# Performance work log

Measured on AMD Instinct MI355X. Metric: run time of the kernel, lower is better.

## Reference

```python
import jax, jax.numpy as jnp
import numpy as np

B, P_SIDE, ENC = 32, 14, 2048
EMB = DEC = ATT = 512
V, L = 10000, 52


def setup_inputs() -> dict:
    key = jax.random.key(0)
    ks = jax.random.split(key, 16)
    u = lambda k, s, a=0.1: jax.random.uniform(k, s, jnp.float32, -a, a)
    return dict(
        image_features=jax.random.normal(ks[0], (B, P_SIDE, P_SIDE, ENC), jnp.float32),
        caption_tokens=jax.random.randint(ks[1], (B, L), 0, V),
        caption_lengths=jax.random.randint(ks[2], (B,), 2, L + 1).at[0].set(L),
        # Attention (init_weights: uniform(-0.1,0.1), zero bias)
        W_enc=u(ks[3], (ATT, ENC)), b_enc=jnp.zeros((ATT,), jnp.float32),
        W_dec=u(ks[4], (ATT, DEC)), b_dec=jnp.zeros((ATT,), jnp.float32),
        w_full=u(ks[5], (ATT,)), b_full=jnp.zeros((), jnp.float32),
        emb_table=u(ks[6], (V, EMB)),
        # LSTMCell (PyTorch gate order i,f,g,o)
        W_ih=u(ks[7], (4 * DEC, EMB + ENC), 0.02), b_ih=jnp.zeros((4 * DEC,), jnp.float32),
        W_hh=u(ks[8], (4 * DEC, DEC), 0.02), b_hh=jnp.zeros((4 * DEC,), jnp.float32),
        W_h0=u(ks[9], (DEC, ENC), 0.02), b_h0=jnp.zeros((DEC,), jnp.float32),
        W_c0=u(ks[10], (DEC, ENC), 0.02), b_c0=jnp.zeros((DEC,), jnp.float32),
        W_beta=u(ks[11], (ENC, DEC), 0.02), b_beta=jnp.zeros((ENC,), jnp.float32),
        W_fc=u(ks[12], (V, DEC), 0.02), b_fc=jnp.zeros((V,), jnp.float32),
    )


def reference(image_features, caption_tokens, caption_lengths,
              W_enc, b_enc, W_dec, b_dec, w_full, b_full, emb_table,
              W_ih, b_ih, W_hh, b_hh, W_h0, b_h0, W_c0, b_c0,
              W_beta, b_beta, W_fc, b_fc):
    bsz = image_features.shape[0]
    enc_dim = image_features.shape[-1]
    img = image_features.reshape(bsz, -1, enc_dim)            # B,P,ENC
    # sort by caption length descending (torch: caption_lengths.sort(descending=True))
    sort_index = jnp.argsort(-caption_lengths)
    lengths = caption_lengths[sort_index]
    img = img[sort_index]
    toks = caption_tokens[sort_index]
    embs = emb_table[toks]                                    # B,L,EMB
    mean_img = img.mean(axis=1)                               # B,ENC
    h0 = mean_img @ W_h0.T + b_h0
    c0 = mean_img @ W_c0.T + b_c0
    decode_lengths = lengths - 1                              # B
    T = toks.shape[1] - 1                                     # static max decode length
    # encoder projection is h-independent: hoist out of the time loop (same math)
    enc_att = jnp.einsum('bpe,ae->bpa', img, W_enc) + b_enc   # B,P,A

    def step(carry, xs):
        h, c = carry
        emb_t, t = xs                                         # emb_t: B,EMB
        # Bahdanau additive attention
        dec_att = h @ W_dec.T + b_dec                         # B,A
        score = jnp.einsum('bpa,a->bp', jax.nn.relu(enc_att + dec_att[:, None, :]), w_full) + b_full
        alpha = jax.nn.softmax(score, axis=1)                 # B,P
        awe = jnp.einsum('bp,bpe->be', alpha, img)            # B,ENC
        gate = jax.nn.sigmoid(h @ W_beta.T + b_beta)
        awe = gate * awe
        # LSTMCell step on [emb; awe]
        x = jnp.concatenate([emb_t, awe], axis=1)
        g = x @ W_ih.T + b_ih + h @ W_hh.T + b_hh
        gi, gf, gg, go = jnp.split(g, 4, axis=1)
        c_new = jax.nn.sigmoid(gf) * c + jax.nn.sigmoid(gi) * jnp.tanh(gg)
        h_new = jax.nn.sigmoid(go) * jnp.tanh(c_new)
        # dynamic batch truncation -> masking (rows with t >= decode_length freeze)
        active = (t < decode_lengths)[:, None]
        h = jnp.where(active, h_new, h)
        c = jnp.where(active, c_new, c)
        preds = jnp.where(active, h_new @ W_fc.T + b_fc, 0.0)  # dropout in eval = identity
        alpha = jnp.where(active, alpha, 0.0)
        return (h, c), (preds, alpha)

    xs = (jnp.swapaxes(embs[:, :T, :], 0, 1), jnp.arange(T))
    (_, _), (preds, alphas) = jax.lax.scan(step, (h0, c0), xs)
    predictions = jnp.swapaxes(preds, 0, 1)                   # B,T,V
    alphas = jnp.swapaxes(alphas, 0, 1)                       # B,T,P
    return predictions, toks, decode_lengths, alphas, sort_index
```

## Files before the change

kernel.cpp:

```cpp
#include <hip/hip_runtime.h>
#include <hip/hip_bf16.h>
#include <cstddef>

#define BB 32
#define PP 196
#define ENCD 2048
#define EMBD 512
#define DECD 512
#define ATTD 512
#define VV 10000
#define LLEN 52
#define TT 51
#define HPC 8
#define GAC 16

#define OFF_PRED  0
#define OFF_TOKS  16320000
#define OFF_DLEN  16321664
#define OFF_ALPHA 16321696
#define OFF_SIDX  16641568

typedef __attribute__((ext_vector_type(8))) short short8;
typedef __attribute__((ext_vector_type(4))) float floatx4;

__device__ __forceinline__ float sigmf(float x) { return 1.0f / (1.0f + __expf(-x)); }
__device__ __forceinline__ unsigned short f2bf(float x) {
    __hip_bfloat16 h = __float2bfloat16(x);
    return *(unsigned short*)&h;
}

__global__ void k_sort(const int* __restrict__ toks, const int* __restrict__ lens,
                       int* __restrict__ sidx, int* __restrict__ dlen, float* __restrict__ out) {
    __shared__ int s_idx[BB];
    if (threadIdx.x == 0) {
        int idx[BB], ln[BB];
        for (int i = 0; i < BB; i++) { idx[i] = i; ln[i] = lens[i]; }
        for (int i = 1; i < BB; i++) {
            int ci = idx[i], cl = ln[i]; int j = i - 1;
            while (j >= 0 && ln[j] < cl) { ln[j + 1] = ln[j]; idx[j + 1] = idx[j]; j--; }
            ln[j + 1] = cl; idx[j + 1] = ci;
        }
        for (int i = 0; i < BB; i++) {
            s_idx[i] = idx[i];
            sidx[i] = idx[i];
            int d = ln[i] - 1;
            dlen[i] = d;
            out[OFF_DLEN + i] = (float)d;
            out[OFF_SIDX + i] = (float)idx[i];
        }
    }
    __syncthreads();
    for (int i = threadIdx.x; i < BB * LLEN; i += blockDim.x) {
        int b = i / LLEN, l = i % LLEN;
        out[OFF_TOKS + i] = (float)toks[s_idx[b] * LLEN + l];
    }
}

__global__ void k_mean(const float* __restrict__ img, const int* __restrict__ sidx,
                       float* __restrict__ meanT) {
    int b = blockIdx.x, ec = blockIdx.y, tid = threadIdx.x;
    int e = ec * 256 + tid;
    const float* ib = img + (size_t)sidx[b] * PP * ENCD + e;
    float acc = 0.f;
#pragma unroll 4
    for (int p = 0; p < PP; p++) acc += ib[(size_t)p * ENCD];
    meanT[(size_t)e * BB + b] = acc * (1.0f / 196.0f);
}

__global__ void k_h0c0(const float* __restrict__ meanT,
                       const float* __restrict__ Wh0, const float* __restrict__ bh0,
                       const float* __restrict__ Wc0, const float* __restrict__ bc0,
                       float* __restrict__ xT, float* __restrict__ c) {
    __shared__ float sx[256 * BB];
    int tid = threadIdx.x;
    int cl = tid >> 3, bq = tid & 7;
    int col = blockIdx.x * 32 + cl;
    const float* wr = (col < 512) ? Wh0 + (size_t)col * ENCD
                                  : Wc0 + (size_t)(col - 512) * ENCD;
    float acc[4] = {0, 0, 0, 0};
    for (int k0 = 0; k0 < ENCD; k0 += 256) {
        __syncthreads();
        for (int i = tid; i < 256 * BB; i += 256) sx[i] = meanT[(size_t)k0 * BB + i];
        __syncthreads();
        for (int k = 0; k < 256; k++) {
            float w = wr[k0 + k];
            const float* x = sx + k * BB + bq * 4;
            acc[0] += w * x[0]; acc[1] += w * x[1]; acc[2] += w * x[2]; acc[3] += w * x[3];
        }
    }
#pragma unroll
    for (int j = 0; j < 4; j++) {
        int b = bq * 4 + j;
        if (col < 512) {
            float v = acc[j] + bh0[col];
            xT[(size_t)(2048 + col) * BB + b] = v;
        } else {
            float v = acc[j] + bc0[col - 512];
            c[b * DECD + (col - 512)] = v;
        }
    }
}

__global__ void k_twh2(const float* __restrict__ Wdec, const float* __restrict__ Wbeta,
                       const float* __restrict__ Whh, float* __restrict__ WhT2) {
    __shared__ float sT[32][33];
    int kt = blockIdx.x, ct = blockIdx.y;
    int tx = threadIdx.x & 31, ty = threadIdx.x >> 5;
    for (int j = 0; j < 4; j++) {
        int cc = ct * 32 + ty + j * 8;
        int kk = kt * 32 + tx;
        float v = (cc < 512) ? Wdec[(size_t)cc * 512 + kk]
                 : (cc < 2560) ? Wbeta[(size_t)(cc - 512) * 512 + kk]
                               : Whh[(size_t)(cc - 2560) * 512 + kk];
        sT[ty + j * 8][tx] = v;
    }
    __syncthreads();
    for (int j = 0; j < 4; j++) {
        int kk = kt * 32 + ty + j * 8;
        int cc = ct * 32 + tx;
        WhT2[(size_t)kk * 4608 + cc] = sT[tx][ty + j * 8];
    }
}

__global__ void k_twg2(const float* __restrict__ Wih, float* __restrict__ WgaT) {
    __shared__ float sT[32][33];
    int kt = blockIdx.x, dt = blockIdx.y;
    int tx = threadIdx.x & 31, ty = threadIdx.x >> 5;
    for (int j = 0; j < 4; j++) {
        int dd = dt * 32 + ty + j * 8;
        int kk = kt * 32 + tx;
        sT[ty + j * 8][tx] = Wih[(size_t)dd * 2560 + 512 + kk];
    }
    __syncthreads();
    for (int j = 0; j < 4; j++) {
        int kk = kt * 32 + ty + j * 8;
        int dd = dt * 32 + tx;
        WgaT[(size_t)kk * 2048 + dd] = sT[tx][ty + j * 8];
    }
}

__global__ void k_cvtfc(const float* __restrict__ Wfc, unsigned int* __restrict__ WfcB) {
    int base = (blockIdx.x * 256 + threadIdx.x) * 4;
    for (int j = 0; j < 4; j++) {
        int ui = base + j;
        const float* src = Wfc + (size_t)ui * 2;
        unsigned int lo = f2bf(src[0]), hi = f2bf(src[1]);
        WfcB[ui] = lo | (hi << 16);
    }
}

__global__ void k_enc(const float* __restrict__ img, const int* __restrict__ sidx,
                      const float* __restrict__ Wenc, const float* __restrict__ benc,
                      float* __restrict__ enc_att) {
    __shared__ float sA[16][68];
    __shared__ float sW[16][132];
    __shared__ size_t sRB[64];
    int mb = blockIdx.x, c0 = blockIdx.y * 128;
    int tid = threadIdx.x;
    int tm = tid >> 5, tn = tid & 31;
    if (tid < 64) {
        int row = mb * 64 + tid;
        int b = row / PP, p = row % PP;
        sRB[tid] = ((size_t)sidx[b] * PP + p) * ENCD;
    }
    __syncthreads();
    float acc[8][4];
#pragma unroll
    for (int i = 0; i < 8; i++)
#pragma unroll
        for (int j = 0; j < 4; j++) acc[i][j] = 0.f;

    for (int kk = 0; kk < ENCD; kk += 16) {
        {
            int m = tid >> 2, kq = tid & 3;
            float4 v = *(const float4*)(img + sRB[m] + kk + kq * 4);
            sA[kq * 4 + 0][m] = v.x; sA[kq * 4 + 1][m] = v.y;
            sA[kq * 4 + 2][m] = v.z; sA[kq * 4 + 3][m] = v.w;
        }
        {
            int nl = tid & 127, kh = tid >> 7;
            const float* wr = Wenc + (size_t)(c0 + nl) * ENCD + kk + kh * 8;
            float4 v0 = *(const float4*)(wr);
            float4 v1 = *(const float4*)(wr + 4);
            sW[kh * 8 + 0][nl] = v0.x; sW[kh * 8 + 1][nl] = v0.y;
            sW[kh * 8 + 2][nl] = v0.z; sW[kh * 8 + 3][nl] = v0.w;
            sW[kh * 8 + 4][nl] = v1.x; sW[kh * 8 + 5][nl] = v1.y;
            sW[kh * 8 + 6][nl] = v1.z; sW[kh * 8 + 7][nl] = v1.w;
        }
        __syncthreads();
#pragma unroll
        for (int k = 0; k < 16; k++) {
            float4 a0 = *(const float4*)&sA[k][tm * 8];
            float4 a1 = *(const float4*)&sA[k][tm * 8 + 4];
            float4 w0 = *(const float4*)&sW[k][tn * 4];
            float av[8] = {a0.x, a0.y, a0.z, a0.w, a1.x, a1.y, a1.z, a1.w};
            float wv[4] = {w0.x, w0.y, w0.z, w0.w};
#pragma unroll
            for (int i = 0; i < 8; i++)
#pragma unroll
                for (int j = 0; j < 4; j++) acc[i][j] += av[i] * wv[j];
        }
        __syncthreads();
    }
#pragma unroll
    for (int i = 0; i < 8; i++) {
        int row = mb * 64 + tm * 8 + i;
        float* orow = enc_att + (size_t)row * ATTD + c0;
        int ca = tn * 4;
        float4 oa = {acc[i][0] + benc[c0 + ca + 0], acc[i][1] + benc[c0 + ca + 1],
                     acc[i][2] + benc[c0 + ca + 2], acc[i][3] + benc[c0 + ca + 3]};
        *(float4*)(orow + ca) = oa;
    }
}

__global__ void k_gemb(const float* __restrict__ emb, const int* __restrict__ toks,
                       const int* __restrict__ sidx, const float* __restrict__ Wih,
                       const float* __restrict__ bih, const float* __restrict__ bhh,
                       float* __restrict__ gbase) {
    __shared__ float As[32][33];
    __shared__ float Ws[32][65];
    __shared__ size_t rb[32];
    int row0 = blockIdx.x * 32, col0 = blockIdx.y * 64;
    int tid = threadIdx.x;
    int tr = tid & 31, tc = tid >> 5;
    if (tid < 32) {
        int t = blockIdx.x, b = tid;
        int tok = toks[sidx[b] * LLEN + t];
        rb[tid] = (size_t)tok * EMBD;
    }
    __syncthreads();
    float acc[8] = {0, 0, 0, 0, 0, 0, 0, 0};
    for (int kk = 0; kk < EMBD; kk += 32) {
        for (int i = tid; i < 1024; i += 256) {
            int r = i >> 5, k = i & 31;
            As[r][k] = emb[rb[r] + kk + k];
        }
        for (int i = tid; i < 2048; i += 256) {
            int cc = i >> 5, k = i & 31;
            Ws[k][cc] = Wih[(size_t)(col0 + cc) * (EMBD + ENCD) + kk + k];
        }
        __syncthreads();
        for (int k = 0; k < 32; k++) {
            float a = As[tr][k];
#pragma unroll
            for (int j = 0; j < 8; j++) acc[j] += a * Ws[k][tc * 8 + j];
        }
        __syncthreads();
    }
    int row = row0 + tr;
    float* crow = gbase + (size_t)row * 2048 + col0 + tc * 8;
#pragma unroll
    for (int j = 0; j < 8; j++) {
        int col = col0 + tc * 8 + j;
        crow[j] = acc[j] + bih[col] + bhh[col];
    }
}

__global__ void k_hproj2(const float* __restrict__ xT, const float* __restrict__ WhT2,
                         float* __restrict__ hp2) {
    int tid = threadIdx.x;
    int cq = tid >> 4, bq = tid & 15;
    int c4 = blockIdx.x * 128 + cq * 4;
    int b2 = bq * 2;
    int k0 = blockIdx.y * 64;
    const float* wp = WhT2 + (size_t)k0 * 4608 + c4;
    const float* xp = xT + (size_t)(2048 + k0) * BB + b2;
    float4 acc0 = make_float4(0.f, 0.f, 0.f, 0.f);
    float4 acc1 = make_float4(0.f, 0.f, 0.f, 0.f);
#pragma unroll 8
    for (int k = 0; k < 64; k++) {
        float4 w = *(const float4*)(wp + (size_t)k * 4608);
        float2 x = *(const float2*)(xp + k * BB);
        acc0.x += x.x * w.x; acc0.y += x.x * w.y; acc0.z += x.x * w.z; acc0.w += x.x * w.w;
        acc1.x += x.y * w.x; acc1.y += x.y * w.y; acc1.z += x.y * w.z; acc1.w += x.y * w.w;
    }
    *(float4*)(hp2 + ((size_t)(blockIdx.y * BB + b2 + 0)) * 4608 + c4) = acc0;
    *(float4*)(hp2 + ((size_t)(blockIdx.y * BB + b2 + 1)) * 4608 + c4) = acc1;
}

__global__ void k_score(const float* __restrict__ hp2, const float* __restrict__ bdec,
                        const float* __restrict__ wfull, const float* __restrict__ enc_att,
                        float* __restrict__ sraw) {
    int b = blockIdx.x, pq = blockIdx.y, tid = threadIdx.x;
    __shared__ float sdec[512], swf[512];
    for (int a = tid; a < 512; a += 256) {
        float v = bdec[a];
#pragma unroll
        for (int kc = 0; kc < HPC; kc++) v += hp2[((size_t)(kc * BB + b)) * 4608 + a];
        sdec[a] = v;
        swf[a] = wfull[a];
    }
    __syncthreads();
    int wv = tid >> 6, ln = tid & 63;
    const float* eb = enc_att + (size_t)b * PP * ATTD;
    const int p0 = pq * 25;
    const int p1 = (p0 + 25 < PP) ? p0 + 25 : PP;
    for (int p = p0 + wv; p < p1; p += 4) {
        const float* er = eb + (size_t)p * ATTD;
        float acc = 0.f;
#pragma unroll
        for (int i = 0; i < 8; i++) {
            int a = ln + i * 64;
            acc += fmaxf(er[a] + sdec[a], 0.f) * swf[a];
        }
#pragma unroll
        for (int off = 32; off; off >>= 1) acc += __shfl_down(acc, off);
        if (ln == 0) sraw[b * 200 + p] = acc;
    }
}

__global__ void k_awe2(int t, const float* __restrict__ img, const int* __restrict__ sidx,
                       const float* __restrict__ sraw, const float* __restrict__ hp2,
                       const float* __restrict__ bbeta, const int* __restrict__ dlen,
                       float* __restrict__ xT, float* __restrict__ out_alpha) {
    int b = blockIdx.x, ec = blockIdx.y, tid = threadIdx.x;
    __shared__ float sal[200], sred[256], sgate[256], sp4[1024];
    __shared__ int ssb;
    if (tid == 0) ssb = sidx[b];
    float v = (tid < PP) ? sraw[b * 200 + tid] : -1e30f;
    sred[tid] = v;
    __syncthreads();
    for (int s = 128; s; s >>= 1) { if (tid < s) sred[tid] = fmaxf(sred[tid], sred[tid + s]); __syncthreads(); }
    float mx = sred[0];
    __syncthreads();
    float e = (tid < PP) ? __expf(v - mx) : 0.f;
    sred[tid] = e;
    __syncthreads();
    for (int s = 128; s; s >>= 1) { if (tid < s) sred[tid] += sred[tid + s]; __syncthreads(); }
    float inv = 1.f / sred[0];
    if (tid < PP) sal[tid] = e * inv;
    {
        int col = 512 + ec * 256 + tid;
        float g = bbeta[ec * 256 + tid];
#pragma unroll
        for (int kc = 0; kc < HPC; kc++) g += hp2[((size_t)(kc * BB + b)) * 4608 + col];
        sgate[tid] = sigmf(g);
    }
    __syncthreads();
    int col4 = tid & 63, pg = tid >> 6;
    const float* ib = img + (size_t)ssb * PP * ENCD + ec * 256 + col4 * 4;
    float4 acc = {0.f, 0.f, 0.f, 0.f};
    const int p0 = pg * 49;
#pragma unroll 7
    for (int p = 0; p < 49; p++) {
        float a = sal[p0 + p];
        float4 vv = *(const float4*)(ib + (size_t)(p0 + p) * ENCD);
        acc.x += a * vv.x; acc.y += a * vv.y; acc.z += a * vv.z; acc.w += a * vv.w;
    }
    *(float4*)(sp4 + tid * 4) = acc;
    __syncthreads();
    if (tid < 64) {
        float4 a0 = *(const float4*)(sp4 + tid * 4);
        float4 a1 = *(const float4*)(sp4 + (64 + tid) * 4);
        float4 a2 = *(const float4*)(sp4 + (128 + tid) * 4);
        float4 a3 = *(const float4*)(sp4 + (192 + tid) * 4);
        int e4 = ec * 256 + tid * 4;
        float r0 = (a0.x + a1.x + a2.x + a3.x) * sgate[tid * 4 + 0];
        float r1 = (a0.y + a1.y + a2.y + a3.y) * sgate[tid * 4 + 1];
        float r2 = (a0.z + a1.z + a2.z + a3.z) * sgate[tid * 4 + 2];
        float r3 = (a0.w + a1.w + a2.w + a3.w) * sgate[tid * 4 + 3];
        xT[(size_t)(e4 + 0) * BB + b] = r0;
        xT[(size_t)(e4 + 1) * BB + b] = r1;
        xT[(size_t)(e4 + 2) * BB + b] = r2;
        xT[(size_t)(e4 + 3) * BB + b] = r3;
    }
    if (ec == 0 && tid < PP) {
        bool act = t < dlen[b];
        out_alpha[((size_t)b * TT + t) * PP + tid] = act ? sal[tid] : 0.f;
    }
}

__global__ void k_gawe(const float* __restrict__ xT, const float* __restrict__ WgaT,
                       float* __restrict__ gpa) {
    int tid = threadIdx.x;
    int dq = tid >> 4, bq = tid & 15;
    int d4 = blockIdx.x * 128 + dq * 4;
    int b2 = bq * 2;
    int k0 = blockIdx.y * 128;
    const float* wp = WgaT + (size_t)k0 * 2048 + d4;
    const float* xp = xT + (size_t)k0 * BB + b2;
    float4 acc0 = make_float4(0.f, 0.f, 0.f, 0.f);
    float4 acc1 = make_float4(0.f, 0.f, 0.f, 0.f);
#pragma unroll 8
    for (int k = 0; k < 128; k++) {
        float4 w = *(const float4*)(wp + (size_t)k * 2048);
        float2 x = *(const float2*)(xp + k * BB);
        acc0.x += x.x * w.x; acc0.y += x.x * w.y; acc0.z += x.x * w.z; acc0.w += x.x * w.w;
        acc1.x += x.y * w.x; acc1.y += x.y * w.y; acc1.z += x.y * w.z; acc1.w += x.y * w.w;
    }
    *(float4*)(gpa + ((size_t)(blockIdx.y * BB + b2 + 0)) * 2048 + d4) = acc0;
    *(float4*)(gpa + ((size_t)(blockIdx.y * BB + b2 + 1)) * 2048 + d4) = acc1;
}

__global__ void k_update2(int t, const float* __restrict__ gbase, const float* __restrict__ hp2,
                          const float* __restrict__ gpa, const int* __restrict__ dlen,
                          float* __restrict__ xT, float* __restrict__ c,
                          unsigned short* __restrict__ hB) {
    int b = blockIdx.x >> 3;
    int d = (blockIdx.x & 7) * 64 + threadIdx.x;
    bool active = t < dlen[b];
    const float* gb = gbase + ((size_t)t * BB + b) * 2048;
    float gs[4];
#pragma unroll
    for (int q = 0; q < 4; q++) {
        int r = d + q * 512;
        float g = gb[r];
#pragma unroll
        for (int kc = 0; kc < HPC; kc++) g += hp2[((size_t)(kc * BB + b)) * 4608 + 2560 + r];
#pragma unroll
        for (int kc = 0; kc < GAC; kc++) g += gpa[((size_t)(kc * BB + b)) * 2048 + r];
        gs[q] = g;
    }
    float i_ = sigmf(gs[0]), f_ = sigmf(gs[1]), g_ = tanhf(gs[2]), o_ = sigmf(gs[3]);
    float cv = c[b * DECD + d];
    float cn = f_ * cv + i_ * g_;
    float hn = o_ * tanhf(cn);
    float hv;
    if (active) { c[b * DECD + d] = cn; xT[(size_t)(2048 + d) * BB + b] = hn; hv = hn; }
    else hv = xT[(size_t)(2048 + d) * BB + b];
    hB[((size_t)t * BB + b) * DECD + d] = f2bf(hv);
}

__global__ void k_pred(const unsigned short* __restrict__ hB, const unsigned short* __restrict__ WfcB,
                       const float* __restrict__ bfc, const int* __restrict__ dlen,
                       float* __restrict__ out) {
    __shared__ unsigned short sA[32 * 40];
    __shared__ unsigned short sB[256 * 40];
    int t = blockIdx.x, n0 = blockIdx.y * 256;
    int tid = threadIdx.x;
    int wv = tid >> 6, lane = tid & 63;
    int quad = lane >> 4, l16 = lane & 15;

    floatx4 acc[2][4];
#pragma unroll
    for (int i = 0; i < 2; i++)
#pragma unroll
        for (int j = 0; j < 4; j++) acc[i][j] = (floatx4){0.f, 0.f, 0.f, 0.f};

    for (int kk = 0; kk < 512; kk += 32) {
        {
            unsigned int* dst = (unsigned int*)sA;
            for (int j = 0; j < 2; j++) {
                int idx = tid + j * 256;
                int m = idx >> 4, kp = idx & 15;
                dst[m * 20 + kp] = ((const unsigned int*)(hB + ((size_t)(t * 32 + m)) * 512 + kk))[kp];
            }
        }
        {
            unsigned int* dst = (unsigned int*)sB;
#pragma unroll
            for (int j = 0; j < 16; j++) {
                int idx = tid + j * 256;
                int n = idx >> 4, kp = idx & 15;
                int gn = n0 + n;
                unsigned int v = 0u;
                if (gn < VV) v = ((const unsigned int*)(WfcB + (size_t)gn * 512 + kk))[kp];
                dst[n * 20 + kp] = v;
            }
        }
        __syncthreads();
        short8 af[2], bf[4];
#pragma unroll
        for (int mt = 0; mt < 2; mt++)
            af[mt] = *(const short8*)(sA + (mt * 16 + l16) * 40 + quad * 8);
#pragma unroll
        for (int nt = 0; nt < 4; nt++) {
            int nl = wv * 64 + nt * 16 + l16;
            bf[nt] = *(const short8*)(sB + nl * 40 + quad * 8);
        }
#pragma unroll
        for (int mt = 0; mt < 2; mt++)
#pragma unroll
            for (int nt = 0; nt < 4; nt++)
                acc[mt][nt] = __builtin_amdgcn_mfma_f32_16x16x32_bf16(af[mt], bf[nt], acc[mt][nt], 0, 0, 0);
        __syncthreads();
    }
#pragma unroll
    for (int mt = 0; mt < 2; mt++) {
#pragma unroll
        for (int r = 0; r < 4; r++) {
            int m = mt * 16 + quad * 4 + r;
            bool active = t < dlen[m];
            float* orow = out + OFF_PRED + ((size_t)m * TT + t) * VV;
#pragma unroll
            for (int nt = 0; nt < 4; nt++) {
                int n = n0 + wv * 64 + nt * 16 + l16;
                if (n < VV) orow[n] = active ? (acc[mt][nt][r] + bfc[n]) : 0.f;
            }
        }
    }
}

extern "C" void kernel_launch(void* const* d_in, const int* in_sizes, int n_in,
                              void* d_out, int out_size, void* d_ws, size_t ws_size,
                              hipStream_t stream) {
    const float* img   = (const float*)d_in[0];
    const int*   toks  = (const int*)d_in[1];
    const int*   lens  = (const int*)d_in[2];
    const float* Wenc  = (const float*)d_in[3];
    const float* benc  = (const float*)d_in[4];
    const float* Wdec  = (const float*)d_in[5];
    const float* bdec  = (const float*)d_in[6];
    const float* wfull = (const float*)d_in[7];
    const float* emb   = (const float*)d_in[9];
    const float* Wih   = (const float*)d_in[10];
    const float* bih   = (const float*)d_in[11];
    const float* Whh   = (const float*)d_in[12];
    const float* bhh   = (const float*)d_in[13];
    const float* Wh0   = (const float*)d_in[14];
    const float* bh0   = (const float*)d_in[15];
    const float* Wc0   = (const float*)d_in[16];
    const float* bc0   = (const float*)d_in[17];
    const float* Wbeta = (const float*)d_in[18];
    const float* bbeta = (const float*)d_in[19];
    const float* Wfc   = (const float*)d_in[20];
    const float* bfc   = (const float*)d_in[21];
    float* out = (float*)d_out;

    char* ws = (char*)d_ws;
    int* sidx = (int*)ws;                  ws += 256;
    int* dlen = (int*)ws;                  ws += 256;
    float* c        = (float*)ws;          ws += (size_t)BB * DECD * 4;
    float* xT       = (float*)ws;          ws += (size_t)2560 * BB * 4;
    float* meanT    = (float*)ws;          ws += (size_t)ENCD * BB * 4;
    float* sraw     = (float*)ws;          ws += (size_t)BB * 200 * 4;
    float* hp2      = (float*)ws;          ws += (size_t)HPC * BB * 4608 * 4;
    float* gpa      = (float*)ws;          ws += (size_t)GAC * BB * 2048 * 4;
    unsigned short* hB = (unsigned short*)ws; ws += (size_t)TT * BB * DECD * 2;
    float* WhT2     = (float*)ws;          ws += (size_t)512 * 4608 * 4;
    float* WgaT     = (float*)ws;          ws += (size_t)2048 * 2048 * 4;
    unsigned int* WfcB = (unsigned int*)ws; ws += (size_t)VV * 512 * 2;
    float* enc_att  = (float*)ws;          ws += (size_t)BB * PP * ATTD * 4;
    float* gbase    = (float*)ws;          ws += (size_t)TT * BB * 2048 * 4;

    k_sort<<<1, 64, 0, stream>>>(toks, lens, sidx, dlen, out);
    k_mean<<<dim3(32, 8), 256, 0, stream>>>(img, sidx, meanT);
    k_h0c0<<<32, 256, 0, stream>>>(meanT, Wh0, bh0, Wc0, bc0, xT, c);
    k_twh2<<<dim3(16, 144), 256, 0, stream>>>(Wdec, Wbeta, Whh, WhT2);
    k_twg2<<<dim3(64, 64), 256, 0, stream>>>(Wih, WgaT);
    k_cvtfc<<<2500, 256, 0, stream>>>(Wfc, WfcB);
    k_enc<<<dim3(98, 4), 256, 0, stream>>>(img, sidx, Wenc, benc, enc_att);
    k_gemb<<<dim3(51, 32), 256, 0, stream>>>(emb, toks, sidx, Wih, bih, bhh, gbase);

    for (int t = 0; t < TT; t++) {
        k_hproj2<<<dim3(36, HPC), 512, 0, stream>>>(xT, WhT2, hp2);
        k_score<<<dim3(32, 8), 256, 0, stream>>>(hp2, bdec, wfull, enc_att, sraw);
        k_awe2<<<dim3(32, 8), 256, 0, stream>>>(t, img, sidx, sraw, hp2, bbeta, dlen,
                                                xT, out + OFF_ALPHA);
        k_gawe<<<dim3(16, GAC), 512, 0, stream>>>(xT, WgaT, gpa);
        k_update2<<<256, 64, 0, stream>>>(t, gbase, hp2, gpa, dlen, xT, c, hB);
    }

    k_pred<<<dim3(TT, 40), 256, 0, stream>>>(hB, (const unsigned short*)WfcB, bfc, dlen, out);
}
```

Baseline: 4.184 ms.

## Fuse LSTM update into gate GEMM via last-block atomic counter; shrink enc tile

Merges the per-step LSTM cell update into the awe-gate GEMM kernel: each column group's split-K blocks bump an atomic counter, and the last one to finish reduces the partial sums and applies the cell update. This drops one kernel launch per time step (51 in all). The column mapping is changed so each dg group holds all four gates for 32 hidden units. Separately, the encoder projection GEMM now uses a 32-row tile with K step 32, which doubles its grid size. The fusion needs threadfences, and the counters are reset in the sort kernel.

```diff
diff --git a/kernel.cpp b/kernel.cpp
--- a/kernel.cpp
+++ b/kernel.cpp
@@ -30,8 +30,10 @@
 }
 
 __global__ void k_sort(const int* __restrict__ toks, const int* __restrict__ lens,
-                       int* __restrict__ sidx, int* __restrict__ dlen, float* __restrict__ out) {
+                       int* __restrict__ sidx, int* __restrict__ dlen, float* __restrict__ out,
+                       unsigned int* __restrict__ cnt) {
     __shared__ int s_idx[BB];
+    if (threadIdx.x < 16) cnt[threadIdx.x] = 0u;
     if (threadIdx.x == 0) {
         int idx[BB], ln[BB];
         for (int i = 0; i < BB; i++) { idx[i] = i; ln[i] = lens[i]; }
@@ -152,59 +154,58 @@
 __global__ void k_enc(const float* __restrict__ img, const int* __restrict__ sidx,
                       const float* __restrict__ Wenc, const float* __restrict__ benc,
                       float* __restrict__ enc_att) {
-    __shared__ float sA[16][68];
-    __shared__ float sW[16][132];
-    __shared__ size_t sRB[64];
+    __shared__ float sA[32][36];
+    __shared__ float sW[32][132];
+    __shared__ size_t sRB[32];
     int mb = blockIdx.x, c0 = blockIdx.y * 128;
     int tid = threadIdx.x;
     int tm = tid >> 5, tn = tid & 31;
-    if (tid < 64) {
-        int row = mb * 64 + tid;
+    if (tid < 32) {
+        int row = mb * 32 + tid;
         int b = row / PP, p = row % PP;
         sRB[tid] = ((size_t)sidx[b] * PP + p) * ENCD;
     }
     __syncthreads();
-    float acc[8][4];
-#pragma unroll
-    for (int i = 0; i < 8; i++)
+    float acc[4][4];
+#pragma unroll
+    for (int i = 0; i < 4; i++)
 #pragma unroll
         for (int j = 0; j < 4; j++) acc[i][j] = 0.f;
 
-    for (int kk = 0; kk < ENCD; kk += 16) {
+    for (int kk = 0; kk < ENCD; kk += 32) {
         {
-            int m = tid >> 2, kq = tid & 3;
+            int m = tid >> 3, kq = tid & 7;
             float4 v = *(const float4*)(img + sRB[m] + kk + kq * 4);
             sA[kq * 4 + 0][m] = v.x; sA[kq * 4 + 1][m] = v.y;
             sA[kq * 4 + 2][m] = v.z; sA[kq * 4 + 3][m] = v.w;
         }
         {
             int nl = tid & 127, kh = tid >> 7;
-            const float* wr = Wenc + (size_t)(c0 + nl) * ENCD + kk + kh * 8;
-            float4 v0 = *(const float4*)(wr);
-            float4 v1 = *(const float4*)(wr + 4);
-            sW[kh * 8 + 0][nl] = v0.x; sW[kh * 8 + 1][nl] = v0.y;
-            sW[kh * 8 + 2][nl] = v0.z; sW[kh * 8 + 3][nl] = v0.w;
-            sW[kh * 8 + 4][nl] = v1.x; sW[kh * 8 + 5][nl] = v1.y;
-            sW[kh * 8 + 6][nl] = v1.z; sW[kh * 8 + 7][nl] = v1.w;
-        }
-        __syncthreads();
-#pragma unroll
-        for (int k = 0; k < 16; k++) {
-            float4 a0 = *(const float4*)&sA[k][tm * 8];
-            float4 a1 = *(const float4*)&sA[k][tm * 8 + 4];
+            const float* wr = Wenc + (size_t)(c0 + nl) * ENCD + kk + kh * 16;
+#pragma unroll
+            for (int j = 0; j < 4; j++) {
+                float4 v = *(const float4*)(wr + j * 4);
+                sW[kh * 16 + j * 4 + 0][nl] = v.x; sW[kh * 16 + j * 4 + 1][nl] = v.y;
+                sW[kh * 16 + j * 4 + 2][nl] = v.z; sW[kh * 16 + j * 4 + 3][nl] = v.w;
+            }
+        }
+        __syncthreads();
+#pragma unroll
+        for (int k = 0; k < 32; k++) {
+            float4 a0 = *(const float4*)&sA[k][tm * 4];
             float4 w0 = *(const float4*)&sW[k][tn * 4];
-            float av[8] = {a0.x, a0.y, a0.z, a0.w, a1.x, a1.y, a1.z, a1.w};
+            float av[4] = {a0.x, a0.y, a0.z, a0.w};
             float wv[4] = {w0.x, w0.y, w0.z, w0.w};
 #pragma unroll
-            for (int i = 0; i < 8; i++)
+            for (int i = 0; i < 4; i++)
 #pragma unroll
                 for (int j = 0; j < 4; j++) acc[i][j] += av[i] * wv[j];
         }
         __syncthreads();
     }
 #pragma unroll
-    for (int i = 0; i < 8; i++) {
-        int row = mb * 64 + tm * 8 + i;
+    for (int i = 0; i < 4; i++) {
+        int row = mb * 32 + tm * 4 + i;
         float* orow = enc_att + (size_t)row * ATTD + c0;
         int ca = tn * 4;
         float4 oa = {acc[i][0] + benc[c0 + ca + 0], acc[i][1] + benc[c0 + ca + 1],
@@ -370,14 +371,18 @@
     }
 }
 
-__global__ void k_gawe(const float* __restrict__ xT, const float* __restrict__ WgaT,
-                       float* __restrict__ gpa) {
+__global__ void k_gawe2(int t, const float* __restrict__ WgaT, float* __restrict__ gpa,
+                        const float* __restrict__ gbase, const float* __restrict__ hp2,
+                        const int* __restrict__ dlen, float* __restrict__ xT,
+                        float* __restrict__ c, unsigned short* __restrict__ hB,
+                        unsigned int* __restrict__ cnt) {
     int tid = threadIdx.x;
-    int dq = tid >> 4, bq = tid & 15;
-    int d4 = blockIdx.x * 128 + dq * 4;
+    int dg = blockIdx.x, kc = blockIdx.y, k0 = kc * 128;
+    int cq = tid >> 4, bq = tid & 15;
+    int g = cq >> 3, q8 = cq & 7;
+    int dcol = g * 512 + dg * 32 + q8 * 4;
     int b2 = bq * 2;
-    int k0 = blockIdx.y * 128;
-    const float* wp = WgaT + (size_t)k0 * 2048 + d4;
+    const float* wp = WgaT + (size_t)k0 * 2048 + dcol;
     const float* xp = xT + (size_t)k0 * BB + b2;
     float4 acc0 = make_float4(0.f, 0.f, 0.f, 0.f);
     float4 acc1 = make_float4(0.f, 0.f, 0.f, 0.f);
@@ -388,37 +393,42 @@
         acc0.x += x.x * w.x; acc0.y += x.x * w.y; acc0.z += x.x * w.z; acc0.w += x.x * w.w;
         acc1.x += x.y * w.x; acc1.y += x.y * w.y; acc1.z += x.y * w.z; acc1.w += x.y * w.w;
     }
-    *(float4*)(gpa + ((size_t)(blockIdx.y * BB + b2 + 0)) * 2048 + d4) = acc0;
-    *(float4*)(gpa + ((size_t)(blockIdx.y * BB + b2 + 1)) * 2048 + d4) = acc1;
-}
-
-__global__ void k_update2(int t, const float* __restrict__ gbase, const float* __restrict__ hp2,
-                          const float* __restrict__ gpa, const int* __restrict__ dlen,
-                          float* __restrict__ xT, float* __restrict__ c,
-                          unsigned short* __restrict__ hB) {
-    int b = blockIdx.x >> 3;
-    int d = (blockIdx.x & 7) * 64 + threadIdx.x;
-    bool active = t < dlen[b];
-    const float* gb = gbase + ((size_t)t * BB + b) * 2048;
-    float gs[4];
-#pragma unroll
-    for (int q = 0; q < 4; q++) {
-        int r = d + q * 512;
-        float g = gb[r];
-#pragma unroll
-        for (int kc = 0; kc < HPC; kc++) g += hp2[((size_t)(kc * BB + b)) * 4608 + 2560 + r];
-#pragma unroll
-        for (int kc = 0; kc < GAC; kc++) g += gpa[((size_t)(kc * BB + b)) * 2048 + r];
-        gs[q] = g;
-    }
-    float i_ = sigmf(gs[0]), f_ = sigmf(gs[1]), g_ = tanhf(gs[2]), o_ = sigmf(gs[3]);
-    float cv = c[b * DECD + d];
-    float cn = f_ * cv + i_ * g_;
-    float hn = o_ * tanhf(cn);
-    float hv;
-    if (active) { c[b * DECD + d] = cn; xT[(size_t)(2048 + d) * BB + b] = hn; hv = hn; }
-    else hv = xT[(size_t)(2048 + d) * BB + b];
-    hB[((size_t)t * BB + b) * DECD + d] = f2bf(hv);
+    *(float4*)(gpa + ((size_t)(kc * BB + b2 + 0)) * 2048 + dcol) = acc0;
+    *(float4*)(gpa + ((size_t)(kc * BB + b2 + 1)) * 2048 + dcol) = acc1;
+    __threadfence();
+    __syncthreads();
+    __shared__ unsigned int s_old;
+    if (tid == 0) s_old = atomicAdd(&cnt[dg], 1u);
+    __syncthreads();
+    if (s_old != GAC - 1) return;
+    __threadfence();
+#pragma unroll
+    for (int r = 0; r < 2; r++) {
+        int o = tid + r * 512;
+        int dl = o & 31, b = o >> 5;
+        int dd = dg * 32 + dl;
+        bool active = t < dlen[b];
+        float gs[4];
+#pragma unroll
+        for (int q = 0; q < 4; q++) {
+            int rr = q * 512 + dd;
+            float gv = gbase[((size_t)t * BB + b) * 2048 + rr];
+#pragma unroll
+            for (int k2 = 0; k2 < HPC; k2++) gv += hp2[((size_t)(k2 * BB + b)) * 4608 + 2560 + rr];
+#pragma unroll
+            for (int k2 = 0; k2 < GAC; k2++) gv += gpa[((size_t)(k2 * BB + b)) * 2048 + rr];
+            gs[q] = gv;
+        }
+        float i_ = sigmf(gs[0]), f_ = sigmf(gs[1]), g_ = tanhf(gs[2]), o_ = sigmf(gs[3]);
+        float cv = c[b * DECD + dd];
+        float cn = f_ * cv + i_ * g_;
+        float hn = o_ * tanhf(cn);
+        float hv;
+        if (active) { c[b * DECD + dd] = cn; xT[(size_t)(2048 + dd) * BB + b] = hn; hv = hn; }
+        else hv = xT[(size_t)(2048 + dd) * BB + b];
+        hB[((size_t)t * BB + b) * DECD + dd] = f2bf(hv);
+    }
+    if (tid == 0) atomicExch(&cnt[dg], 0u);
 }
 
 __global__ void k_pred(const unsigned short* __restrict__ hB, const unsigned short* __restrict__ WfcB,
@@ -520,6 +530,7 @@
     char* ws = (char*)d_ws;
     int* sidx = (int*)ws;                  ws += 256;
     int* dlen = (int*)ws;                  ws += 256;
+    unsigned int* cnt = (unsigned int*)ws; ws += 256;
     float* c        = (float*)ws;          ws += (size_t)BB * DECD * 4;
     float* xT       = (float*)ws;          ws += (size_t)2560 * BB * 4;
     float* meanT    = (float*)ws;          ws += (size_t)ENCD * BB * 4;
@@ -533,13 +544,13 @@
     float* enc_att  = (float*)ws;          ws += (size_t)BB * PP * ATTD * 4;
     float* gbase    = (float*)ws;          ws += (size_t)TT * BB * 2048 * 4;
 
-    k_sort<<<1, 64, 0, stream>>>(toks, lens, sidx, dlen, out);
+    k_sort<<<1, 64, 0, stream>>>(toks, lens, sidx, dlen, out, cnt);
     k_mean<<<dim3(32, 8), 256, 0, stream>>>(img, sidx, meanT);
     k_h0c0<<<32, 256, 0, stream>>>(meanT, Wh0, bh0, Wc0, bc0, xT, c);
     k_twh2<<<dim3(16, 144), 256, 0, stream>>>(Wdec, Wbeta, Whh, WhT2);
     k_twg2<<<dim3(64, 64), 256, 0, stream>>>(Wih, WgaT);
     k_cvtfc<<<2500, 256, 0, stream>>>(Wfc, WfcB);
-    k_enc<<<dim3(98, 4), 256, 0, stream>>>(img, sidx, Wenc, benc, enc_att);
+    k_enc<<<dim3(196, 4), 256, 0, stream>>>(img, sidx, Wenc, benc, enc_att);
     k_gemb<<<dim3(51, 32), 256, 0, stream>>>(emb, toks, sidx, Wih, bih, bhh, gbase);
 
     for (int t = 0; t < TT; t++) {
@@ -547,8 +558,8 @@
         k_score<<<dim3(32, 8), 256, 0, stream>>>(hp2, bdec, wfull, enc_att, sraw);
         k_awe2<<<dim3(32, 8), 256, 0, stream>>>(t, img, sidx, sraw, hp2, bbeta, dlen,
                                                 xT, out + OFF_ALPHA);
-        k_gawe<<<dim3(16, GAC), 512, 0, stream>>>(xT, WgaT, gpa);
-        k_update2<<<256, 64, 0, stream>>>(t, gbase, hp2, gpa, dlen, xT, c, hB);
+        k_gawe2<<<dim3(16, GAC), 512, 0, stream>>>(t, WgaT, gpa, gbase, hp2, dlen,
+                                                   xT, c, hB, cnt);
     }
 
     k_pred<<<dim3(TT, 40), 256, 0, stream>>>(hB, (const unsigned short*)WfcB, bfc, dlen, out);
```

Measured after the change: 7.285 ms. +74.1%, slower.

## Merge independent setup kernels into one block-dispatched mega kernel

Applied to the files above, without the earlier changes.

Folds six independent preprocessing kernels (encoder projection, h0/c0 init, embedding gate GEMM, two weight transposes, FC bf16 conversion) into a single launch whose block index picks the task. This removes five launch gaps and lets the small, latency-bound tasks fill CUs alongside the heavy encoder GEMM. The cost is one shared-memory allocation sized for the largest branch, which may lower occupancy for the lighter branches, and the per-timestep loop is left unchanged.

```diff
diff --git a/kernel.cpp b/kernel.cpp
--- a/kernel.cpp
+++ b/kernel.cpp
@@ -20,6 +20,14 @@
 #define OFF_ALPHA 16321696
 #define OFF_SIDX  16641568
 
+#define MB_ENC   392
+#define MB_H0C0  (MB_ENC + 32)
+#define MB_GEMB  (MB_H0C0 + 1632)
+#define MB_TWH2  (MB_GEMB + 2304)
+#define MB_TWG2  (MB_TWH2 + 4096)
+#define MB_CVT   (MB_TWG2 + 2500)
+#define MB_TOTAL MB_CVT
+
 typedef __attribute__((ext_vector_type(8))) short short8;
 typedef __attribute__((ext_vector_type(4))) float floatx4;
 
@@ -67,192 +75,190 @@
     meanT[(size_t)e * BB + b] = acc * (1.0f / 196.0f);
 }
 
-__global__ void k_h0c0(const float* __restrict__ meanT,
+__global__ void k_mega(const float* __restrict__ img, const int* __restrict__ sidx,
+                       const float* __restrict__ Wenc, const float* __restrict__ benc,
+                       float* __restrict__ enc_att,
+                       const float* __restrict__ meanT,
                        const float* __restrict__ Wh0, const float* __restrict__ bh0,
                        const float* __restrict__ Wc0, const float* __restrict__ bc0,
-                       float* __restrict__ xT, float* __restrict__ c) {
-    __shared__ float sx[256 * BB];
-    int tid = threadIdx.x;
-    int cl = tid >> 3, bq = tid & 7;
-    int col = blockIdx.x * 32 + cl;
-    const float* wr = (col < 512) ? Wh0 + (size_t)col * ENCD
-                                  : Wc0 + (size_t)(col - 512) * ENCD;
-    float acc[4] = {0, 0, 0, 0};
-    for (int k0 = 0; k0 < ENCD; k0 += 256) {
+                       float* __restrict__ xT, float* __restrict__ c,
+                       const float* __restrict__ emb, const int* __restrict__ toks,
+                       const float* __restrict__ Wih, const float* __restrict__ bih,
+                       const float* __restrict__ bhh, float* __restrict__ gbase,
+                       const float* __restrict__ Wdec, const float* __restrict__ Wbeta,
+                       const float* __restrict__ Whh, float* __restrict__ WhT2,
+                       float* __restrict__ WgaT,
+                       const float* __restrict__ Wfc, unsigned int* __restrict__ WfcB) {
+    __shared__ float S[8192];
+    int bid = blockIdx.x, tid = threadIdx.x;
+
+    if (bid < MB_ENC) {
+        float* sA = S;
+        float* sW = S + 16 * 68;
+        size_t* sRB = (size_t*)(S + 16 * 68 + 16 * 132);
+        int mb = bid >> 2, c0 = (bid & 3) * 128;
+        int tm = tid >> 5, tn = tid & 31;
+        if (tid < 64) {
+            int row = mb * 64 + tid;
+            int b = row / PP, p = row % PP;
+            sRB[tid] = ((size_t)sidx[b] * PP + p) * ENCD;
+        }
         __syncthreads();
-        for (int i = tid; i < 256 * BB; i += 256) sx[i] = meanT[(size_t)k0 * BB + i];
+        float acc[8][4];
+#pragma unroll
+        for (int i = 0; i < 8; i++)
+#pragma unroll
+            for (int j = 0; j < 4; j++) acc[i][j] = 0.f;
+        for (int kk = 0; kk < ENCD; kk += 16) {
+            {
+                int m = tid >> 2, kq = tid & 3;
+                float4 v = *(const float4*)(img + sRB[m] + kk + kq * 4);
+                sA[(kq * 4 + 0) * 68 + m] = v.x; sA[(kq * 4 + 1) * 68 + m] = v.y;
+                sA[(kq * 4 + 2) * 68 + m] = v.z; sA[(kq * 4 + 3) * 68 + m] = v.w;
+            }
+            {
+                int nl = tid & 127, kh = tid >> 7;
+                const float* wr = Wenc + (size_t)(c0 + nl) * ENCD + kk + kh * 8;
+                float4 v0 = *(const float4*)(wr);
+                float4 v1 = *(const float4*)(wr + 4);
+                sW[(kh * 8 + 0) * 132 + nl] = v0.x; sW[(kh * 8 + 1) * 132 + nl] = v0.y;
+                sW[(kh * 8 + 2) * 132 + nl] = v0.z; sW[(kh * 8 + 3) * 132 + nl] = v0.w;
+                sW[(kh * 8 + 4) * 132 + nl] = v1.x; sW[(kh * 8 + 5) * 132 + nl] = v1.y;
+                sW[(kh * 8 + 6) * 132 + nl] = v1.z; sW[(kh * 8 + 7) * 132 + nl] = v1.w;
+            }
+            __syncthreads();
+#pragma unroll
+            for (int k = 0; k < 16; k++) {
+                float4 a0 = *(const float4*)&sA[k * 68 + tm * 8];
+                float4 a1 = *(const float4*)&sA[k * 68 + tm * 8 + 4];
+                float4 w0 = *(const float4*)&sW[k * 132 + tn * 4];
+                float av[8] = {a0.x, a0.y, a0.z, a0.w, a1.x, a1.y, a1.z, a1.w};
+                float wv[4] = {w0.x, w0.y, w0.z, w0.w};
+#pragma unroll
+                for (int i = 0; i < 8; i++)
+#pragma unroll
+                    for (int j = 0; j < 4; j++) acc[i][j] += av[i] * wv[j];
+            }
+            __syncthreads();
+        }
+#pragma unroll
+        for (int i = 0; i < 8; i++) {
+            int row = mb * 64 + tm * 8 + i;
+            float* orow = enc_att + (size_t)row * ATTD + c0;
+            int ca = tn * 4;
+            float4 oa = {acc[i][0] + benc[c0 + ca + 0], acc[i][1] + benc[c0 + ca + 1],
+                         acc[i][2] + benc[c0 + ca + 2], acc[i][3] + benc[c0 + ca + 3]};
+            *(float4*)(orow + ca) = oa;
+        }
+    } else if (bid < MB_H0C0) {
+        float* sx = S;
+        int blk = bid - MB_ENC;
+        int cl = tid >> 3, bq = tid & 7;
+        int col = blk * 32 + cl;
+        const float* wr = (col < 512) ? Wh0 + (size_t)col * ENCD
+                                      : Wc0 + (size_t)(col - 512) * ENCD;
+        float acc[4] = {0, 0, 0, 0};
+        for (int k0 = 0; k0 < ENCD; k0 += 256) {
+            __syncthreads();
+            for (int i = tid; i < 256 * BB; i += 256) sx[i] = meanT[(size_t)k0 * BB + i];
+            __syncthreads();
+            for (int k = 0; k < 256; k++) {
+                float w = wr[k0 + k];
+                const float* x = sx + k * BB + bq * 4;
+                acc[0] += w * x[0]; acc[1] += w * x[1]; acc[2] += w * x[2]; acc[3] += w * x[3];
+            }
+        }
+#pragma unroll
+        for (int j = 0; j < 4; j++) {
+            int b = bq * 4 + j;
+            if (col < 512) {
+                xT[(size_t)(2048 + col) * BB + b] = acc[j] + bh0[col];
+            } else {
+                c[b * DECD + (col - 512)] = acc[j] + bc0[col - 512];
+            }
+        }
+    } else if (bid < MB_GEMB) {
+        float* As = S;
+        float* Ws = S + 32 * 33;
+        size_t* rb = (size_t*)(S + 32 * 33 + 32 * 65);
+        int blk = bid - MB_H0C0;
+        int tblk = blk >> 5, yb = blk & 31;
+        int row0 = tblk * 32, col0 = yb * 64;
+        int tr = tid & 31, tc = tid >> 5;
+        if (tid < 32) {
+            int tok = toks[sidx[tid] * LLEN + tblk];
+            rb[tid] = (size_t)tok * EMBD;
+        }
         __syncthreads();
-        for (int k = 0; k < 256; k++) {
-            float w = wr[k0 + k];
-            const float* x = sx + k * BB + bq * 4;
-            acc[0] += w * x[0]; acc[1] += w * x[1]; acc[2] += w * x[2]; acc[3] += w * x[3];
-        }
-    }
-#pragma unroll
-    for (int j = 0; j < 4; j++) {
-        int b = bq * 4 + j;
-        if (col < 512) {
-            float v = acc[j] + bh0[col];
-            xT[(size_t)(2048 + col) * BB + b] = v;
-        } else {
-            float v = acc[j] + bc0[col - 512];
-            c[b * DECD + (col - 512)] = v;
-        }
-    }
-}
-
-__global__ void k_twh2(const float* __restrict__ Wdec, const float* __restrict__ Wbeta,
-                       const float* __restrict__ Whh, float* __restrict__ WhT2) {
-    __shared__ float sT[32][33];
-    int kt = blockIdx.x, ct = blockIdx.y;
-    int tx = threadIdx.x & 31, ty = threadIdx.x >> 5;
-    for (int j = 0; j < 4; j++) {
-        int cc = ct * 32 + ty + j * 8;
-        int kk = kt * 32 + tx;
-        float v = (cc < 512) ? Wdec[(size_t)cc * 512 + kk]
-                 : (cc < 2560) ? Wbeta[(size_t)(cc - 512) * 512 + kk]
-                               : Whh[(size_t)(cc - 2560) * 512 + kk];
-        sT[ty + j * 8][tx] = v;
-    }
-    __syncthreads();
-    for (int j = 0; j < 4; j++) {
-        int kk = kt * 32 + ty + j * 8;
-        int cc = ct * 32 + tx;
-        WhT2[(size_t)kk * 4608 + cc] = sT[tx][ty + j * 8];
-    }
-}
-
-__global__ void k_twg2(const float* __restrict__ Wih, float* __restrict__ WgaT) {
-    __shared__ float sT[32][33];
-    int kt = blockIdx.x, dt = blockIdx.y;
-    int tx = threadIdx.x & 31, ty = threadIdx.x >> 5;
-    for (int j = 0; j < 4; j++) {
-        int dd = dt * 32 + ty + j * 8;
-        int kk = kt * 32 + tx;
-        sT[ty + j * 8][tx] = Wih[(size_t)dd * 2560 + 512 + kk];
-    }
-    __syncthreads();
-    for (int j = 0; j < 4; j++) {
-        int kk = kt * 32 + ty + j * 8;
-        int dd = dt * 32 + tx;
-        WgaT[(size_t)kk * 2048 + dd] = sT[tx][ty + j * 8];
-    }
-}
-
-__global__ void k_cvtfc(const float* __restrict__ Wfc, unsigned int* __restrict__ WfcB) {
-    int base = (blockIdx.x * 256 + threadIdx.x) * 4;
-    for (int j = 0; j < 4; j++) {
-        int ui = base + j;
-        const float* src = Wfc + (size_t)ui * 2;
-        unsigned int lo = f2bf(src[0]), hi = f2bf(src[1]);
-        WfcB[ui] = lo | (hi << 16);
-    }
-}
-
-__global__ void k_enc(const float* __restrict__ img, const int* __restrict__ sidx,
-                      const float* __restrict__ Wenc, const float* __restrict__ benc,
-                      float* __restrict__ enc_att) {
-    __shared__ float sA[16][68];
-    __shared__ float sW[16][132];
-    __shared__ size_t sRB[64];
-    int mb = blockIdx.x, c0 = blockIdx.y * 128;
-    int tid = threadIdx.x;
-    int tm = tid >> 5, tn = tid & 31;
-    if (tid < 64) {
-        int row = mb * 64 + tid;
-        int b = row / PP, p = row % PP;
-        sRB[tid] = ((size_t)sidx[b] * PP + p) * ENCD;
-    }
-    __syncthreads();
-    float acc[8][4];
-#pragma unroll
-    for (int i = 0; i < 8; i++)
-#pragma unroll
-        for (int j = 0; j < 4; j++) acc[i][j] = 0.f;
-
-    for (int kk = 0; kk < ENCD; kk += 16) {
-        {
-            int m = tid >> 2, kq = tid & 3;
-            float4 v = *(const float4*)(img + sRB[m] + kk + kq * 4);
-            sA[kq * 4 + 0][m] = v.x; sA[kq * 4 + 1][m] = v.y;
-            sA[kq * 4 + 2][m] = v.z; sA[kq * 4 + 3][m] = v.w;
-        }
-        {
-            int nl = tid & 127, kh = tid >> 7;
-            const float* wr = Wenc + (size_t)(c0 + nl) * ENCD + kk + kh * 8;
-            float4 v0 = *(const float4*)(wr);
-            float4 v1 = *(const float4*)(wr + 4);
-            sW[kh * 8 + 0][nl] = v0.x; sW[kh * 8 + 1][nl] = v0.y;
-            sW[kh * 8 + 2][nl] = v0.z; sW[kh * 8 + 3][nl] = v0.w;
-            sW[kh * 8 + 4][nl] = v1.x; sW[kh * 8 + 5][nl] = v1.y;
-            sW[kh * 8 + 6][nl] = v1.z; sW[kh * 8 + 7][nl] = v1.w;
+        float acc[8] = {0, 0, 0, 0, 0, 0, 0, 0};
+        for (int kk = 0; kk < EMBD; kk += 32) {
+            for (int i = tid; i < 1024; i += 256) {
+                int r = i >> 5, k = i & 31;
+                As[r * 33 + k] = emb[rb[r] + kk + k];
+            }
+            for (int i = tid; i < 2048; i += 256) {
+                int cc = i >> 5, k = i & 31;
+                Ws[k * 65 + cc] = Wih[(size_t)(col0 + cc) * (EMBD + ENCD) + kk + k];
+            }
+            __syncthreads();
+            for (int k = 0; k < 32; k++) {
+                float a = As[tr * 33 + k];
+#pragma unroll
+                for (int j = 0; j < 8; j++) acc[j] += a * Ws[k * 65 + tc * 8 + j];
+            }
+            __syncthreads();
+        }
+        int row = row0 + tr;
+        float* crow = gbase + (size_t)row * 2048 + col0 + tc * 8;
+#pragma unroll
+        for (int j = 0; j < 8; j++) {
+            int col = col0 + tc * 8 + j;
+            crow[j] = acc[j] + bih[col] + bhh[col];
+        }
+    } else if (bid < MB_TWH2) {
+        float* sT = S;
+        int blk = bid - MB_GEMB;
+        int kt = blk & 15, ct = blk >> 4;
+        int tx = tid & 31, ty = tid >> 5;
+        for (int j = 0; j < 4; j++) {
+            int cc = ct * 32 + ty + j * 8;
+            int kk = kt * 32 + tx;
+            float v = (cc < 512) ? Wdec[(size_t)cc * 512 + kk]
+                     : (cc < 2560) ? Wbeta[(size_t)(cc - 512) * 512 + kk]
+                                   : Whh[(size_t)(cc - 2560) * 512 + kk];
+            sT[(ty + j * 8) * 33 + tx] = v;
         }
         __syncthreads();
-#pragma unroll
-        for (int k = 0; k < 16; k++) {
-            float4 a0 = *(const float4*)&sA[k][tm * 8];
-            float4 a1 = *(const float4*)&sA[k][tm * 8 + 4];
-            float4 w0 = *(const float4*)&sW[k][tn * 4];
-            float av[8] = {a0.x, a0.y, a0.z, a0.w, a1.x, a1.y, a1.z, a1.w};
-            float wv[4] = {w0.x, w0.y, w0.z, w0.w};
-#pragma unroll
-            for (int i = 0; i < 8; i++)
-#pragma unroll
-                for (int j = 0; j < 4; j++) acc[i][j] += av[i] * wv[j];
+        for (int j = 0; j < 4; j++) {
+            int kk = kt * 32 + ty + j * 8;
+            int cc = ct * 32 + tx;
+            WhT2[(size_t)kk * 4608 + cc] = sT[tx * 33 + ty + j * 8];
+        }
+    } else if (bid < MB_TWG2) {
+        float* sT = S;
+        int blk = bid - MB_TWH2;
+        int kt = blk & 63, dt = blk >> 6;
+        int tx = tid & 31, ty = tid >> 5;
+        for (int j = 0; j < 4; j++) {
+            int dd = dt * 32 + ty + j * 8;
+            int kk = kt * 32 + tx;
+            sT[(ty + j * 8) * 33 + tx] = Wih[(size_t)dd * 2560 + 512 + kk];
         }
         __syncthreads();
-    }
-#pragma unroll
-    for (int i = 0; i < 8; i++) {
-        int row = mb * 64 + tm * 8 + i;
-        float* orow = enc_att + (size_t)row * ATTD + c0;
-        int ca = tn * 4;
-        float4 oa = {acc[i][0] + benc[c0 + ca + 0], acc[i][1] + benc[c0 + ca + 1],
-                     acc[i][2] + benc[c0 + ca + 2], acc[i][3] + benc[c0 + ca + 3]};
-        *(float4*)(orow + ca) = oa;
-    }
-}
-
-__global__ void k_gemb(const float* __restrict__ emb, const int* __restrict__ toks,
-                       const int* __restrict__ sidx, const float* __restrict__ Wih,
-                       const float* __restrict__ bih, const float* __restrict__ bhh,
-                       float* __restrict__ gbase) {
-    __shared__ float As[32][33];
-    __shared__ float Ws[32][65];
-    __shared__ size_t rb[32];
-    int row0 = blockIdx.x * 32, col0 = blockIdx.y * 64;
-    int tid = threadIdx.x;
-    int tr = tid & 31, tc = tid >> 5;
-    if (tid < 32) {
-        int t = blockIdx.x, b = tid;
-        int tok = toks[sidx[b] * LLEN + t];
-        rb[tid] = (size_t)tok * EMBD;
-    }
-    __syncthreads();
-    float acc[8] = {0, 0, 0, 0, 0, 0, 0, 0};
-    for (int kk = 0; kk < EMBD; kk += 32) {
-        for (int i = tid; i < 1024; i += 256) {
-            int r = i >> 5, k = i & 31;
-            As[r][k] = emb[rb[r] + kk + k];
-        }
-        for (int i = tid; i < 2048; i += 256) {
-            int cc = i >> 5, k = i & 31;
-            Ws[k][cc] = Wih[(size_t)(col0 + cc) * (EMBD + ENCD) + kk + k];
-        }
-        __syncthreads();
-        for (int k = 0; k < 32; k++) {
-            float a = As[tr][k];
-#pragma unroll
-            for (int j = 0; j < 8; j++) acc[j] += a * Ws[k][tc * 8 + j];
-        }
-        __syncthreads();
-    }
-    int row = row0 + tr;
-    float* crow = gbase + (size_t)row * 2048 + col0 + tc * 8;
-#pragma unroll
-    for (int j = 0; j < 8; j++) {
-        int col = col0 + tc * 8 + j;
-        crow[j] = acc[j] + bih[col] + bhh[col];
+        for (int j = 0; j < 4; j++) {
+            int kk = kt * 32 + ty + j * 8;
+            int dd = dt * 32 + tx;
+            WgaT[(size_t)kk * 2048 + dd] = sT[tx * 33 + ty + j * 8];
+        }
+    } else {
+        int blk = bid - MB_TWG2;
+        int base = (blk * 256 + tid) * 4;
+        for (int j = 0; j < 4; j++) {
+            int ui = base + j;
+            const float* src = Wfc + (size_t)ui * 2;
+            unsigned int lo = f2bf(src[0]), hi = f2bf(src[1]);
+            WfcB[ui] = lo | (hi << 16);
+        }
     }
 }
 
@@ -535,12 +541,11 @@
 
     k_sort<<<1, 64, 0, stream>>>(toks, lens, sidx, dlen, out);
     k_mean<<<dim3(32, 8), 256, 0, stream>>>(img, sidx, meanT);
-    k_h0c0<<<32, 256, 0, stream>>>(meanT, Wh0, bh0, Wc0, bc0, xT, c);
-    k_twh2<<<dim3(16, 144), 256, 0, stream>>>(Wdec, Wbeta, Whh, WhT2);
-    k_twg2<<<dim3(64, 64), 256, 0, stream>>>(Wih, WgaT);
-    k_cvtfc<<<2500, 256, 0, stream>>>(Wfc, WfcB);
-    k_enc<<<dim3(98, 4), 256, 0, stream>>>(img, sidx, Wenc, benc, enc_att);
-    k_gemb<<<dim3(51, 32), 256, 0, stream>>>(emb, toks, sidx, Wih, bih, bhh, gbase);
+    k_mega<<<MB_TOTAL, 256, 0, stream>>>(img, sidx, Wenc, benc, enc_att,
+                                         meanT, Wh0, bh0, Wc0, bc0, xT, c,
+                                         emb, toks, Wih, bih, bhh, gbase,
+                                         Wdec, Wbeta, Whh, WhT2, WgaT,
+                                         Wfc, WfcB);
 
     for (int t = 0; t < TT; t++) {
         k_hproj2<<<dim3(36, HPC), 512, 0, stream>>>(xT, WhT2, hp2);
```

New measurement: 3.898 ms. -6.8%, faster.
